# Performance work log

Hardware: AMD Instinct MI355X
Metric: run time of the kernel (lower is better)

The kernel has to match this reference:

```python
import jax, jax.numpy as jnp
import numpy as np


def setup_inputs() -> dict:
    key = jax.random.key(0)
    k1, k2 = jax.random.split(key)
    # x: (batch=16, channels=256, window=64, n_patches=128)
    x = jax.random.normal(k1, (16, 256, 64, 128), dtype=jnp.float32)
    # codebooks: (nsubq=4, codebook_size=2**(num_bits//2)=256, sub_channels=64)
    codebooks = jax.random.normal(k2, (4, 256, 64), dtype=jnp.float32)
    return {"x": x, "codebooks": codebooks}


def reference(x, codebooks):
    B, C, W, P = x.shape
    ns, K, sc = codebooks.shape  # ns=4, K=256, sc=C//ns
    # split channels into nsubq subspaces: (B, ns, sc, W, P) -> (ns, B*W*P, sc)
    xs = x.reshape(B, ns, sc, W, P).transpose(1, 0, 3, 4, 2).reshape(ns, B * W * P, sc)
    # squared euclidean distances (argmin identical to cdist argmin)
    d2 = (jnp.sum(xs * xs, axis=-1, keepdims=True)
          - 2.0 * jnp.einsum('snc,skc->snk', xs, codebooks)
          + jnp.sum(codebooks * codebooks, axis=-1)[:, None, :])  # (ns, N, K)
    idx = jnp.argmin(d2, axis=-1)  # (ns, N)
    q = jnp.take_along_axis(codebooks, idx[:, :, None], axis=1)  # (ns, N, sc)
    # faithful to the torch code: data was flattened in (B, W, P) order but
    # view()'d back as (B, P, W) -- reshape reproduces that reinterpretation
    q = q.reshape(ns, B, P, W, sc).transpose(1, 2, 3, 0, 4).reshape(B, P, W, C)
    # final permute(0, 3, 2, 1) -> (B, C, W, P)
    return q.transpose(0, 3, 2, 1)
```

## Files before the change

### kernel.cpp

```cpp
#include <hip/hip_runtime.h>

#define NSQ 4
#define KCB 256
#define SCH 64
#define BB  16
#define WW  64
#define PP  128
#define NVEC (BB*WW*PP)
#define TILES_PER_BLOCK 8
#define BLOCKS_PER_S (NVEC/64/TILES_PER_BLOCK)

__global__ __launch_bounds__(256) void pq_pass1(const float* __restrict__ x,
                                                const float* __restrict__ cb,
                                                int* __restrict__ idx_out)
{
    __shared__ float cbt[64][256];
    const int tid = threadIdx.x;
    const int s   = blockIdx.x >> 8;
    const int blk = blockIdx.x & (BLOCKS_PER_S - 1);
    const int tk  = tid & 15;
    const int tn  = tid >> 4;
    const int swz = ((tk ^ (tk >> 2)) & 3) << 2;

    {
        const int k    = tid;
        const int tks  = k >> 4;
        const int swzs = ((tks ^ (tks >> 2)) & 3) << 2;
        const int col  = (k & ~15) | ((k & 15) ^ swzs);
        const float* row = cb + (size_t)(s * KCB + k) * SCH;
#pragma unroll
        for (int j4 = 0; j4 < 16; ++j4) {
            float4 v = *(const float4*)(row + j4 * 4);
            cbt[j4*4 + 0][col] = v.x;
            cbt[j4*4 + 1][col] = v.y;
            cbt[j4*4 + 2][col] = v.z;
            cbt[j4*4 + 3][col] = v.w;
        }
    }
    __syncthreads();

    const int cb0 = (tk << 4) | (0  ^ swz);
    const int cb1 = (tk << 4) | (4  ^ swz);
    const int cb2 = (tk << 4) | (8  ^ swz);
    const int cb3 = (tk << 4) | (12 ^ swz);

    float cn[16];
#pragma unroll
    for (int kk = 0; kk < 16; ++kk) cn[kk] = 0.f;
    for (int j = 0; j < 64; ++j) {
        float c[16];
        {
            float4 t0 = *(const float4*)&cbt[j][cb0];
            float4 t1 = *(const float4*)&cbt[j][cb1];
            float4 t2 = *(const float4*)&cbt[j][cb2];
            float4 t3 = *(const float4*)&cbt[j][cb3];
            c[0]=t0.x; c[1]=t0.y; c[2]=t0.z; c[3]=t0.w;
            c[4]=t1.x; c[5]=t1.y; c[6]=t1.z; c[7]=t1.w;
            c[8]=t2.x; c[9]=t2.y; c[10]=t2.z; c[11]=t2.w;
            c[12]=t3.x; c[13]=t3.y; c[14]=t3.z; c[15]=t3.w;
        }
#pragma unroll
        for (int kk = 0; kk < 16; ++kk) cn[kk] = fmaf(c[kk], c[kk], cn[kk]);
    }

    for (int t = 0; t < TILES_PER_BLOCK; ++t) {
        const int n_base = blk * (TILES_PER_BLOCK * 64) + t * 64;
        const int b  = n_base >> 13;
        const int w  = (n_base >> 7) & 63;
        const int p0 = n_base & 127;
        const float* xp = x + ((size_t)((b * 256 + s * 64) * 64 + w)) * 128 + p0 + 4 * tn;

        float acc[4][16];
#pragma unroll
        for (int nn = 0; nn < 4; ++nn)
#pragma unroll
            for (int kk = 0; kk < 16; ++kk) acc[nn][kk] = 0.f;

#pragma unroll 2
        for (int j = 0; j < 64; ++j) {
            float4 xv = *(const float4*)(xp + (size_t)j * 8192);
            float c[16];
            {
                float4 t0 = *(const float4*)&cbt[j][cb0];
                float4 t1 = *(const float4*)&cbt[j][cb1];
                float4 t2 = *(const float4*)&cbt[j][cb2];
                float4 t3 = *(const float4*)&cbt[j][cb3];
                c[0]=t0.x; c[1]=t0.y; c[2]=t0.z; c[3]=t0.w;
                c[4]=t1.x; c[5]=t1.y; c[6]=t1.z; c[7]=t1.w;
                c[8]=t2.x; c[9]=t2.y; c[10]=t2.z; c[11]=t2.w;
                c[12]=t3.x; c[13]=t3.y; c[14]=t3.z; c[15]=t3.w;
            }
#pragma unroll
            for (int kk = 0; kk < 16; ++kk) {
                acc[0][kk] = fmaf(xv.x, c[kk], acc[0][kk]);
                acc[1][kk] = fmaf(xv.y, c[kk], acc[1][kk]);
                acc[2][kk] = fmaf(xv.z, c[kk], acc[2][kk]);
                acc[3][kk] = fmaf(xv.w, c[kk], acc[3][kk]);
            }
        }

        float best[4] = {3.4e38f, 3.4e38f, 3.4e38f, 3.4e38f};
        int   bidx[4] = {0, 0, 0, 0};
#pragma unroll
        for (int kk = 0; kk < 16; ++kk) {
            const int k = (tk << 4) + kk;
#pragma unroll
            for (int nn = 0; nn < 4; ++nn) {
                float d = fmaf(-2.f, acc[nn][kk], cn[kk]);
                bool better = (d < best[nn]);
                best[nn] = better ? d : best[nn];
                bidx[nn] = better ? k : bidx[nn];
            }
        }
#pragma unroll
        for (int m = 8; m; m >>= 1) {
#pragma unroll
            for (int nn = 0; nn < 4; ++nn) {
                float ob = __shfl_xor(best[nn], m, 64);
                int   oi = __shfl_xor(bidx[nn], m, 64);
                bool take = (ob < best[nn]) || (ob == best[nn] && oi < bidx[nn]);
                best[nn] = take ? ob : best[nn];
                bidx[nn] = take ? oi : bidx[nn];
            }
        }
        if (tk == 0) {
            int4 r; r.x = bidx[0]; r.y = bidx[1]; r.z = bidx[2]; r.w = bidx[3];
            *(int4*)(idx_out + (size_t)s * NVEC + n_base + 4 * tn) = r;
        }
    }
}

__global__ __launch_bounds__(256) void pq_pass2(const float* __restrict__ cb,
                                                const int* __restrict__ idx,
                                                float* __restrict__ out)
{
    __shared__ int   L[64][132];
    __shared__ float cbc[256];
    const int tid = threadIdx.x;
    const int bc  = blockIdx.x;
    const int b   = bc >> 8;
    const int c   = bc & 255;
    const int s   = c >> 6;
    const int j   = c & 63;

    cbc[tid] = cb[(size_t)(s * KCB + tid) * SCH + j];

    const int* ip = idx + (size_t)s * NVEC + b * 8192;
#pragma unroll
    for (int r = 0; r < 32; ++r) {
        int g = r * 256 + tid;
        L[g & 63][g >> 6] = ip[g];
    }
    __syncthreads();

    float* op = out + (size_t)bc * 8192;
#pragma unroll
    for (int r = 0; r < 8; ++r) {
        int e4  = (r * 256 + tid) * 4;
        int w_o = e4 >> 7;
        int p_o = e4 & 127;
        int4 kv = *(const int4*)&L[w_o][p_o];
        float4 v;
        v.x = cbc[kv.x];
        v.y = cbc[kv.y];
        v.z = cbc[kv.z];
        v.w = cbc[kv.w];
        *(float4*)(op + e4) = v;
    }
}

extern "C" void kernel_launch(void* const* d_in, const int* in_sizes, int n_in,
                              void* d_out, int out_size, void* d_ws, size_t ws_size,
                              hipStream_t stream) {
    (void)in_sizes; (void)n_in; (void)out_size; (void)ws_size;
    const float* x   = (const float*)d_in[0];
    const float* cbk = (const float*)d_in[1];
    float*       out = (float*)d_out;
    int*         idx = (int*)d_ws;

    pq_pass1<<<NSQ * BLOCKS_PER_S, 256, 0, stream>>>(x, cbk, idx);
    pq_pass2<<<BB * 256, 256, 0, stream>>>(cbk, idx, out);
}
```

Measured before the change: 583.5 us.

## Precompute codebook norms, enlarge pass1 blocks with x prefetch, retile pass2 gather

Codebook norms move into a separate small kernel whose output sits temporarily in the output buffer, so pass1 no longer recomputes them in every block. Pass1 now runs 512-thread blocks that each handle 128 vectors per tile, halving the block count and the number of codebook staging passes into LDS. It also software-prefetches the next x row, including across tile boundaries. Pass2 is restructured so each block stages a 32-column codebook slice and a 64x64 index tile in padded LDS and writes 32 output channels, which reuses index loads across channels but adds LDS gathers with possible bank conflicts.

```diff
diff --git a/kernel.cpp b/kernel.cpp
--- a/kernel.cpp
+++ b/kernel.cpp
@@ -3,30 +3,40 @@
 #define NSQ 4
 #define KCB 256
 #define SCH 64
-#define BB  16
-#define WW  64
-#define PP  128
-#define NVEC (BB*WW*PP)
-#define TILES_PER_BLOCK 8
-#define BLOCKS_PER_S (NVEC/64/TILES_PER_BLOCK)
-
-__global__ __launch_bounds__(256) void pq_pass1(const float* __restrict__ x,
-                                                const float* __restrict__ cb,
-                                                int* __restrict__ idx_out)
+#define NVEC (16*64*128)
+
+__global__ void pq_norms(const float* __restrict__ cb, float* __restrict__ cn)
+{
+    const int s = blockIdx.x, k = threadIdx.x;
+    const float* row = cb + (size_t)(s * KCB + k) * SCH;
+    float n = 0.f;
+#pragma unroll
+    for (int j4 = 0; j4 < 16; ++j4) {
+        float4 v = *(const float4*)(row + j4 * 4);
+        n = fmaf(v.x, v.x, n); n = fmaf(v.y, v.y, n);
+        n = fmaf(v.z, v.z, n); n = fmaf(v.w, v.w, n);
+    }
+    cn[s * KCB + k] = n;
+}
+
+__global__ __launch_bounds__(512, 4) void pq_pass1(const float* __restrict__ x,
+                                                   const float* __restrict__ cb,
+                                                   const float* __restrict__ cnorm,
+                                                   int* __restrict__ idx_out)
 {
     __shared__ float cbt[64][256];
     const int tid = threadIdx.x;
-    const int s   = blockIdx.x >> 8;
-    const int blk = blockIdx.x & (BLOCKS_PER_S - 1);
+    const int s   = blockIdx.x >> 7;
+    const int blk = blockIdx.x & 127;
     const int tk  = tid & 15;
     const int tn  = tid >> 4;
     const int swz = ((tk ^ (tk >> 2)) & 3) << 2;
 
-    {
+    if (tid < 256) {
         const int k    = tid;
         const int tks  = k >> 4;
-        const int swzs = ((tks ^ (tks >> 2)) & 3) << 2;
-        const int col  = (k & ~15) | ((k & 15) ^ swzs);
+        const int szs  = ((tks ^ (tks >> 2)) & 3) << 2;
+        const int col  = (k & ~15) | ((k & 15) ^ szs);
         const float* row = cb + (size_t)(s * KCB + k) * SCH;
 #pragma unroll
         for (int j4 = 0; j4 < 16; ++j4) {
@@ -43,33 +53,14 @@
     const int cb1 = (tk << 4) | (4  ^ swz);
     const int cb2 = (tk << 4) | (8  ^ swz);
     const int cb3 = (tk << 4) | (12 ^ swz);
-
-    float cn[16];
-#pragma unroll
-    for (int kk = 0; kk < 16; ++kk) cn[kk] = 0.f;
-    for (int j = 0; j < 64; ++j) {
-        float c[16];
-        {
-            float4 t0 = *(const float4*)&cbt[j][cb0];
-            float4 t1 = *(const float4*)&cbt[j][cb1];
-            float4 t2 = *(const float4*)&cbt[j][cb2];
-            float4 t3 = *(const float4*)&cbt[j][cb3];
-            c[0]=t0.x; c[1]=t0.y; c[2]=t0.z; c[3]=t0.w;
-            c[4]=t1.x; c[5]=t1.y; c[6]=t1.z; c[7]=t1.w;
-            c[8]=t2.x; c[9]=t2.y; c[10]=t2.z; c[11]=t2.w;
-            c[12]=t3.x; c[13]=t3.y; c[14]=t3.z; c[15]=t3.w;
-        }
-#pragma unroll
-        for (int kk = 0; kk < 16; ++kk) cn[kk] = fmaf(c[kk], c[kk], cn[kk]);
-    }
-
-    for (int t = 0; t < TILES_PER_BLOCK; ++t) {
-        const int n_base = blk * (TILES_PER_BLOCK * 64) + t * 64;
-        const int b  = n_base >> 13;
-        const int w  = (n_base >> 7) & 63;
-        const int p0 = n_base & 127;
-        const float* xp = x + ((size_t)((b * 256 + s * 64) * 64 + w)) * 128 + p0 + 4 * tn;
-
+    const float* cnp = cnorm + s * KCB + (tk << 4);
+
+    int n_base = blk * 1024;
+    const float* xp = x + ((size_t)(((n_base >> 13) * 256 + s * 64) * 64 +
+                                    ((n_base >> 7) & 63))) * 128 + 4 * tn;
+    float4 xv = *(const float4*)xp;
+
+    for (int t = 0; t < 8; ++t) {
         float acc[4][16];
 #pragma unroll
         for (int nn = 0; nn < 4; ++nn)
@@ -77,8 +68,8 @@
             for (int kk = 0; kk < 16; ++kk) acc[nn][kk] = 0.f;
 
 #pragma unroll 2
-        for (int j = 0; j < 64; ++j) {
-            float4 xv = *(const float4*)(xp + (size_t)j * 8192);
+        for (int j = 0; j < 63; ++j) {
+            float4 xn = *(const float4*)(xp + (size_t)(j + 1) * 8192);
             float c[16];
             {
                 float4 t0 = *(const float4*)&cbt[j][cb0];
@@ -97,16 +88,45 @@
                 acc[2][kk] = fmaf(xv.z, c[kk], acc[2][kk]);
                 acc[3][kk] = fmaf(xv.w, c[kk], acc[3][kk]);
             }
+            xv = xn;
+        }
+        {
+            const int nb2 = blk * 1024 + (t < 7 ? (t + 1) : t) * 128;
+            const float* xp2 = x + ((size_t)(((nb2 >> 13) * 256 + s * 64) * 64 +
+                                             ((nb2 >> 7) & 63))) * 128 + 4 * tn;
+            float4 xnext = *(const float4*)xp2;
+
+            float c[16];
+            {
+                float4 t0 = *(const float4*)&cbt[63][cb0];
+                float4 t1 = *(const float4*)&cbt[63][cb1];
+                float4 t2 = *(const float4*)&cbt[63][cb2];
+                float4 t3 = *(const float4*)&cbt[63][cb3];
+                c[0]=t0.x; c[1]=t0.y; c[2]=t0.z; c[3]=t0.w;
+                c[4]=t1.x; c[5]=t1.y; c[6]=t1.z; c[7]=t1.w;
+                c[8]=t2.x; c[9]=t2.y; c[10]=t2.z; c[11]=t2.w;
+                c[12]=t3.x; c[13]=t3.y; c[14]=t3.z; c[15]=t3.w;
+            }
+#pragma unroll
+            for (int kk = 0; kk < 16; ++kk) {
+                acc[0][kk] = fmaf(xv.x, c[kk], acc[0][kk]);
+                acc[1][kk] = fmaf(xv.y, c[kk], acc[1][kk]);
+                acc[2][kk] = fmaf(xv.z, c[kk], acc[2][kk]);
+                acc[3][kk] = fmaf(xv.w, c[kk], acc[3][kk]);
+            }
+            xv = xnext;
+            xp = xp2;
         }
 
         float best[4] = {3.4e38f, 3.4e38f, 3.4e38f, 3.4e38f};
         int   bidx[4] = {0, 0, 0, 0};
 #pragma unroll
         for (int kk = 0; kk < 16; ++kk) {
+            const float cn = cnp[kk];
             const int k = (tk << 4) + kk;
 #pragma unroll
             for (int nn = 0; nn < 4; ++nn) {
-                float d = fmaf(-2.f, acc[nn][kk], cn[kk]);
+                float d = fmaf(-2.f, acc[nn][kk], cn);
                 bool better = (d < best[nn]);
                 best[nn] = better ? d : best[nn];
                 bidx[nn] = better ? k : bidx[nn];
@@ -127,45 +147,56 @@
             int4 r; r.x = bidx[0]; r.y = bidx[1]; r.z = bidx[2]; r.w = bidx[3];
             *(int4*)(idx_out + (size_t)s * NVEC + n_base + 4 * tn) = r;
         }
-    }
-}
-
-__global__ __launch_bounds__(256) void pq_pass2(const float* __restrict__ cb,
+        n_base += 128;
+    }
+}
+
+__global__ __launch_bounds__(512) void pq_pass2(const float* __restrict__ cb,
                                                 const int* __restrict__ idx,
                                                 float* __restrict__ out)
 {
-    __shared__ int   L[64][132];
-    __shared__ float cbc[256];
+    __shared__ int   L[64][65];
+    __shared__ float cbs[256][33];
     const int tid = threadIdx.x;
-    const int bc  = blockIdx.x;
-    const int b   = bc >> 8;
-    const int c   = bc & 255;
-    const int s   = c >> 6;
-    const int j   = c & 63;
-
-    cbc[tid] = cb[(size_t)(s * KCB + tid) * SCH + j];
-
-    const int* ip = idx + (size_t)s * NVEC + b * 8192;
-#pragma unroll
-    for (int r = 0; r < 32; ++r) {
-        int g = r * 256 + tid;
-        L[g & 63][g >> 6] = ip[g];
+    const int bid = blockIdx.x;
+    const int ph  = bid & 1;
+    const int jh  = (bid >> 1) & 1;
+    const int s   = (bid >> 2) & 3;
+    const int b   = bid >> 4;
+    const int p0  = ph * 64;
+    const int j0  = jh * 32;
+
+    const int* ip = idx + (size_t)s * NVEC + b * 8192 + p0 * 64;
+#pragma unroll
+    for (int it = 0; it < 8; ++it) {
+        int t = it * 512 + tid;
+        L[t & 63][t >> 6] = ip[t];
+    }
+    const float* cp = cb + (size_t)s * (KCB * SCH) + j0;
+#pragma unroll
+    for (int it = 0; it < 4; ++it) {
+        int t = it * 512 + tid;
+        int k = t >> 3, jj4 = (t & 7) * 4;
+        float4 v = *(const float4*)(cp + (size_t)k * SCH + jj4);
+        cbs[k][jj4 + 0] = v.x; cbs[k][jj4 + 1] = v.y;
+        cbs[k][jj4 + 2] = v.z; cbs[k][jj4 + 3] = v.w;
     }
     __syncthreads();
 
-    float* op = out + (size_t)bc * 8192;
-#pragma unroll
-    for (int r = 0; r < 8; ++r) {
-        int e4  = (r * 256 + tid) * 4;
-        int w_o = e4 >> 7;
-        int p_o = e4 & 127;
-        int4 kv = *(const int4*)&L[w_o][p_o];
-        float4 v;
-        v.x = cbc[kv.x];
-        v.y = cbc[kv.y];
-        v.z = cbc[kv.z];
-        v.w = cbc[kv.w];
-        *(float4*)(op + e4) = v;
+    for (int cc = 0; cc < 32; ++cc) {
+        const int c = s * 64 + j0 + cc;
+        float* op = out + ((size_t)(b * 256 + c) * 64) * 128 + p0;
+#pragma unroll
+        for (int q = 0; q < 2; ++q) {
+            int ch = q * 512 + tid;
+            int w  = ch >> 4, pp = (ch & 15) * 4;
+            float4 v;
+            v.x = cbs[L[w][pp + 0]][cc];
+            v.y = cbs[L[w][pp + 1]][cc];
+            v.z = cbs[L[w][pp + 2]][cc];
+            v.w = cbs[L[w][pp + 3]][cc];
+            *(float4*)(op + (size_t)w * 128 + pp) = v;
+        }
     }
 }
 
@@ -177,7 +208,9 @@
     const float* cbk = (const float*)d_in[1];
     float*       out = (float*)d_out;
     int*         idx = (int*)d_ws;
-
-    pq_pass1<<<NSQ * BLOCKS_PER_S, 256, 0, stream>>>(x, cbk, idx);
-    pq_pass2<<<BB * 256, 256, 0, stream>>>(cbk, idx, out);
-}
+    float*       cnrm = (float*)d_out;
+
+    pq_norms<<<NSQ, KCB, 0, stream>>>(cbk, cnrm);
+    pq_pass1<<<NSQ * 128, 512, 0, stream>>>(x, cbk, cnrm, idx);
+    pq_pass2<<<16 * NSQ * 2 * 2, 512, 0, stream>>>(cbk, idx, out);
+}
```

After: 1.516 ms. +159.8%, slower.
